# Optimization experiments

Measured on AMD Instinct MI355X. Metric: run time of the kernel, lower is better.

The kernel has to match this reference:

```python
import jax, jax.numpy as jnp
import numpy as np

IN_CH = 64
EMBED = 128
OUT_CH = 64
NUM_HEADS = 2
HEAD_DIM = EMBED // NUM_HEADS
B, D, H, W = 2, 16, 16, 16
SEQ = D * H * W


def setup_inputs() -> dict:
    key = jax.random.key(0)
    ks = jax.random.split(key, 12)
    s = lambda fan_in: 1.0 / np.sqrt(fan_in)
    return {
        "x": jax.random.normal(ks[0], (B, IN_CH, D, H, W), dtype=jnp.float32),
        "W_cp": jax.random.uniform(ks[1], (EMBED, IN_CH), jnp.float32, -s(IN_CH), s(IN_CH)),
        "b_cp": jax.random.uniform(ks[2], (EMBED,), jnp.float32, -s(IN_CH), s(IN_CH)),
        "W_q": jax.random.uniform(ks[3], (EMBED, EMBED), jnp.float32, -s(EMBED), s(EMBED)),
        "W_k": jax.random.uniform(ks[4], (EMBED, EMBED), jnp.float32, -s(EMBED), s(EMBED)),
        "W_v": jax.random.uniform(ks[5], (EMBED, EMBED), jnp.float32, -s(EMBED), s(EMBED)),
        "W_o": jax.random.uniform(ks[6], (EMBED, EMBED), jnp.float32, -s(EMBED), s(EMBED)),
        "b_o": jax.random.uniform(ks[7], (EMBED,), jnp.float32, -s(EMBED), s(EMBED)),
        "W_out": jax.random.uniform(ks[8], (OUT_CH, EMBED), jnp.float32, -s(EMBED), s(EMBED)),
        "b_out": jax.random.uniform(ks[9], (OUT_CH,), jnp.float32, -s(EMBED), s(EMBED)),
        "pos": jax.random.normal(ks[10], (1, SEQ, EMBED), dtype=jnp.float32) * 0.02,
        "gate": jnp.float32(0.1),
    }


def reference(x, W_cp, b_cp, W_q, W_k, W_v, W_o, b_o, W_out, b_out, pos, gate):
    b, c, d, h, w = x.shape
    seq = d * h * w
    scale = HEAD_DIM ** (-0.5)
    # (B, C, D, H, W) -> (B, S, C)
    xf = jnp.transpose(x, (0, 2, 3, 4, 1)).reshape(b, seq, c)
    xf = xf @ W_cp.T + b_cp + pos  # (B, S, E)
    # QKV projections, split heads: (B, nh, S, hd)
    def heads(t):
        return jnp.transpose(t.reshape(b, seq, NUM_HEADS, HEAD_DIM), (0, 2, 1, 3))
    q = heads(xf @ W_q.T)
    k = heads(xf @ W_k.T)
    v = heads(xf @ W_v.T)
    attn = jax.nn.softmax(jnp.einsum("bnsd,bntd->bnst", q, k) * scale, axis=-1)
    o = jnp.einsum("bnst,bntd->bnsd", attn, v)  # (B, nh, S, hd)
    o = jnp.transpose(o, (0, 2, 1, 3)).reshape(b, seq, EMBED)
    o = o @ W_o.T + b_o
    o = o @ W_out.T + b_out  # (B, S, out)
    out = jnp.transpose(o, (0, 2, 1)).reshape(b, OUT_CH, d, h, w)
    # in_channels == output_dim -> skip is identity (no conv/BN in original)
    return out + gate * x
```

## Files before the change

kernel.cpp:

```cpp
#include <hip/hip_runtime.h>
#include <hip/hip_bf16.h>
#include <cstdint>

typedef unsigned short u16;
typedef __attribute__((ext_vector_type(8))) short short8;
typedef __attribute__((ext_vector_type(4))) float f32x4;

#define MFMA(a, b, c) __builtin_amdgcn_mfma_f32_16x16x32_bf16((a), (b), (c), 0, 0, 0)

#define SEQ 4096
#define KSPLIT 8
#define NTILE (SEQ / KSPLIT / 32)

static __device__ __forceinline__ float b2f(u16 u) {
    union { float f; uint32_t i; } c; c.i = ((uint32_t)u) << 16; return c.f;
}
static __device__ __forceinline__ u16 f2b(float f) {
    union { float f; uint32_t i; } c; c.f = f;
    uint32_t r = c.i + 0x7FFF + ((c.i >> 16) & 1);
    return (u16)(r >> 16);
}
static __device__ __forceinline__ short8 ld8(const u16* p) {
    return *reinterpret_cast<const short8*>(p);
}
static __device__ __forceinline__ uint32_t pk2(float a, float b) {
    uint32_t r;
    asm("v_cvt_pk_bf16_f32 %0, %1, %2" : "=v"(r) : "v"(a), "v"(b));
    return r;
}
static __device__ __forceinline__ void gld16(const u16* g, u16* l) {
    __builtin_amdgcn_global_load_lds(
        (const __attribute__((address_space(1))) unsigned int*)g,
        (__attribute__((address_space(3))) unsigned int*)l, 16, 0, 0);
}

__global__ void k_prep(const float* __restrict__ Wo, const float* __restrict__ bo,
                       const float* __restrict__ Wout, const float* __restrict__ bout,
                       const float* __restrict__ Wcp, const float* __restrict__ Wq,
                       const float* __restrict__ Wk, const float* __restrict__ Wv,
                       u16* __restrict__ Wc, float* __restrict__ bc,
                       u16* __restrict__ Wcp_b, u16* __restrict__ Wq_b,
                       u16* __restrict__ Wk_b, u16* __restrict__ Wv_b) {
    int idx = blockIdx.x * 256 + threadIdx.x;
    if (idx < 8192) {
        int co = idx >> 7, e = idx & 127;
        float s = 0.f;
        for (int k = 0; k < 128; k++)
            s += Wout[co * 128 + k] * Wo[k * 128 + e];
        Wc[idx] = f2b(s);
    } else if (idx < 8256) {
        int co = idx - 8192;
        float s = bout[co];
        for (int k = 0; k < 128; k++)
            s += bo[k] * Wout[co * 128 + k];
        bc[co] = s;
    } else if (idx < 16448) {
        int i = idx - 8256;  Wcp_b[i] = f2b(Wcp[i]);
    } else if (idx < 32832) {
        int i = idx - 16448; Wq_b[i] = f2b(Wq[i]);
    } else if (idx < 49216) {
        int i = idx - 32832; Wk_b[i] = f2b(Wk[i]);
    } else if (idx < 65600) {
        int i = idx - 49216; Wv_b[i] = f2b(Wv[i]);
    }
}

__global__ __launch_bounds__(256) void k_front(const float* __restrict__ x,
                                               const u16* __restrict__ Wcp,
                                               const float* __restrict__ bcp,
                                               const float* __restrict__ pos,
                                               const u16* __restrict__ Wq,
                                               const u16* __restrict__ Wk,
                                               const u16* __restrict__ Wv,
                                               u16* __restrict__ Q, u16* __restrict__ K,
                                               u16* __restrict__ V) {
    __shared__ __align__(16) u16 xT[16][72];
    __shared__ __align__(16) u16 xfl[16 * 128];
    int blk = blockIdx.x;
    int b = blk >> 8, sb = (blk & 255) * 16;
    int t = threadIdx.x, w = t >> 6, l = t & 63, lc = l & 15, lg = l >> 4;

    {
        int c = t & 63, so = t >> 6;
        const float* src = x + ((size_t)b * 64 + c) * SEQ + sb + so * 4;
        f32x4 a0 = *reinterpret_cast<const f32x4*>(src);
#pragma unroll
        for (int j = 0; j < 4; j++) xT[so * 4 + j][c] = f2b(a0[j]);
    }
    __syncthreads();

    {
        short8 af[2];
        af[0] = ld8(&xT[lc][lg * 8]);
        af[1] = ld8(&xT[lc][32 + lg * 8]);
#pragma unroll
        for (int et = 0; et < 2; et++) {
            int nt = w * 2 + et;
            f32x4 acc = {0.f, 0.f, 0.f, 0.f};
#pragma unroll
            for (int ks = 0; ks < 2; ks++) {
                short8 bfr = ld8(Wcp + (nt * 16 + lc) * 64 + ks * 32 + lg * 8);
                acc = MFMA(af[ks], bfr, acc);
            }
            int e = nt * 16 + lc;
            float be = bcp[e];
            int chunk = e >> 3;
#pragma unroll
            for (int r = 0; r < 4; r++) {
                int sl = lg * 4 + r;
                float v = acc[r] + be + pos[(size_t)(sb + sl) * 128 + e];
                xfl[sl * 128 + ((chunk ^ (sl & 7)) << 3) + (e & 7)] = f2b(v);
            }
        }
    }
    __syncthreads();

    {
        short8 afq[4];
#pragma unroll
        for (int ks = 0; ks < 4; ks++)
            afq[ks] = ld8(&xfl[lc * 128 + (((ks * 4 + lg) ^ (lc & 7)) << 3)]);

        const float qscl = 0.18033688011112042f;
#pragma unroll
        for (int qk = 0; qk < 2; qk++) {
            const u16* W = qk ? Wk : Wq;
            u16* dst = qk ? K : Q;
#pragma unroll
            for (int et = 0; et < 2; et++) {
                int nt = w * 2 + et;
                f32x4 acc = {0.f, 0.f, 0.f, 0.f};
#pragma unroll
                for (int ks = 0; ks < 4; ks++) {
                    short8 bfr = ld8(W + (nt * 16 + lc) * 128 + ks * 32 + lg * 8);
                    acc = MFMA(afq[ks], bfr, acc);
                }
                int e = nt * 16 + lc, h = e >> 6, d = e & 63;
                float scl = qk ? 1.0f : qscl;
#pragma unroll
                for (int r = 0; r < 4; r++) {
                    int sr = sb + lg * 4 + r;
                    dst[(((size_t)b * 2 + h) * SEQ + sr) * 64 + d] = f2b(acc[r] * scl);
                }
            }
        }
#pragma unroll
        for (int et = 0; et < 2; et++) {
            int nt = w * 2 + et;
            f32x4 acc = {0.f, 0.f, 0.f, 0.f};
            short8 wv[4];
#pragma unroll
            for (int ks = 0; ks < 4; ks++)
                wv[ks] = ld8(Wv + (nt * 16 + lc) * 128 + ks * 32 + lg * 8);
#pragma unroll
            for (int ks = 0; ks < 4; ks++)
                acc = MFMA(wv[ks], afq[ks], acc);
#pragma unroll
            for (int r = 0; r < 4; r++) {
                int d = nt * 16 + lg * 4 + r, h = d >> 6, dd = d & 63;
                V[((size_t)(b * 2 + h) * 64 + dd) * SEQ + sb + lc] = f2b(acc[r]);
            }
        }
    }
}

__global__ __launch_bounds__(256, 4) void k_attn(const u16* __restrict__ Q,
                                                 const u16* __restrict__ K,
                                                 const u16* __restrict__ Vg,
                                                 u16* __restrict__ Op,
                                                 float2* __restrict__ ml) {
    __shared__ __align__(16) u16 Klds[2][2048];
    __shared__ __align__(16) u16 Vlds[2][2048];
    __shared__ __align__(16) u16 Pl[4][32][32];
    int blk = blockIdx.x;
    int split = blk >> 7, bh = (blk >> 5) & 3, qb = (blk & 31) * 128;
    int kbase = split * (SEQ / KSPLIT);
    const u16* Qp = Q + (size_t)bh * SEQ * 64;
    const u16* Kp = K + (size_t)bh * SEQ * 64;
    const u16* Vp = Vg + (size_t)bh * SEQ * 64;
    int t = threadIdx.x, w = t >> 6, l = t & 63, lc = l & 15, lg = l >> 4;
    uint32_t* plw = (uint32_t*)&Pl[w][0][0];
    const u16* plu = &Pl[w][0][0];

    const u16* kSrc = Kp + (size_t)(kbase + w * 8 + (l >> 3)) * 64 + (((l & 7) ^ (l >> 3)) << 3);
    int vrow = w * 16 + (l >> 2);
    int vswz = (l & 3) ^ ((((l >> 2) & 3) + (l >> 4)) & 3);
    const u16* vSrc = Vp + (size_t)vrow * SEQ + kbase + (vswz << 3);

    short8 qa[2][2];
#pragma unroll
    for (int ks = 0; ks < 2; ks++)
#pragma unroll
        for (int qh = 0; qh < 2; qh++)
            qa[ks][qh] = ld8(Qp + (size_t)(qb + w * 32 + qh * 16 + lc) * 64 + ks * 32 + lg * 8);

    short8 onesb;
#pragma unroll
    for (int i = 0; i < 8; i++) onesb[i] = (short)0x3F80;

    f32x4 oacc[2][4], lsacc[2];
#pragma unroll
    for (int qh = 0; qh < 2; qh++) {
        lsacc[qh] = (f32x4){0.f, 0.f, 0.f, 0.f};
#pragma unroll
        for (int dt = 0; dt < 4; dt++) oacc[qh][dt] = (f32x4){0.f, 0.f, 0.f, 0.f};
    }
    float m[2] = {-INFINITY, -INFINITY};

    int c0 = (lg ^ (lc & 7)) * 8;
    int sp = (((lc & 3) + (lc >> 2)) & 3);
    int cv = (lg ^ sp) * 8;

#define STAGE(buf, tt) do {                                       \
        gld16(kSrc + (size_t)(tt) * 2048, &Klds[buf][w * 512]);   \
        gld16(vSrc + (tt) * 32,           &Vlds[buf][w * 512]);   \
    } while (0)

    STAGE(0, 0);
    __syncthreads();

#pragma unroll 2
    for (int tt = 0; tt < NTILE; tt++) {
        int cur = tt & 1;
        if (tt + 1 < NTILE) STAGE(cur ^ 1, tt + 1);

        const u16* kb = Klds[cur];
        const u16* vb = Vlds[cur];

        f32x4 sc[2][2];
#pragma unroll
        for (int nt = 0; nt < 2; nt++) {
            short8 kf0 = ld8(kb + (nt * 16 + lc) * 64 + c0);
            short8 kf1 = ld8(kb + (nt * 16 + lc) * 64 + (c0 ^ 32));
#pragma unroll
            for (int qh = 0; qh < 2; qh++) {
                f32x4 a = {0.f, 0.f, 0.f, 0.f};
                a = MFMA(kf0, qa[0][qh], a);
                a = MFMA(kf1, qa[1][qh], a);
                sc[nt][qh] = a;
            }
        }

        float mx[2];
#pragma unroll
        for (int qh = 0; qh < 2; qh++)
            mx[qh] = fmaxf(
                fmaxf(fmaxf(sc[0][qh][0], sc[0][qh][1]), fmaxf(sc[0][qh][2], sc[0][qh][3])),
                fmaxf(fmaxf(sc[1][qh][0], sc[1][qh][1]), fmaxf(sc[1][qh][2], sc[1][qh][3])));

        if (__any((mx[0] - m[0] > 8.f) || (mx[1] - m[1] > 8.f))) {
#pragma unroll
            for (int qh = 0; qh < 2; qh++) {
                float mr = fmaxf(mx[qh], __shfl_xor(mx[qh], 16));
                mr = fmaxf(mr, __shfl_xor(mr, 32));
                float mn = fmaxf(m[qh], mr);
                float corr = exp2f(m[qh] - mn);
#pragma unroll
                for (int r = 0; r < 4; r++) {
                    float cr = __shfl(corr, lg * 4 + r);
#pragma unroll
                    for (int dt = 0; dt < 4; dt++) oacc[qh][dt][r] *= cr;
                    lsacc[qh][r] *= cr;
                }
                m[qh] = mn;
            }
        }

#pragma unroll
        for (int qh = 0; qh < 2; qh++) {
            int rowb = (qh * 16 + lc) * 16 + (lg & 1) * 2;
#pragma unroll
            for (int nt = 0; nt < 2; nt++) {
                uint2 u;
                u.x = pk2(exp2f(sc[nt][qh][0] - m[qh]), exp2f(sc[nt][qh][1] - m[qh]));
                u.y = pk2(exp2f(sc[nt][qh][2] - m[qh]), exp2f(sc[nt][qh][3] - m[qh]));
                int cc = (nt * 2 + (lg >> 1)) ^ sp;
                *reinterpret_cast<uint2*>(&plw[rowb + cc * 4]) = u;
            }
        }

        short8 pa0 = ld8(plu + (lc) * 32 + cv);
        short8 pa1 = ld8(plu + (16 + lc) * 32 + cv);
        lsacc[0] = MFMA(pa0, onesb, lsacc[0]);
        lsacc[1] = MFMA(pa1, onesb, lsacc[1]);
#pragma unroll
        for (int dt = 0; dt < 4; dt++) {
            short8 vf = ld8(vb + (dt * 16 + lc) * 32 + cv);
            oacc[0][dt] = MFMA(pa0, vf, oacc[0][dt]);
            oacc[1][dt] = MFMA(pa1, vf, oacc[1][dt]);
        }
        __syncthreads();
    }
#undef STAGE

    size_t rowbase = (size_t)(split * 4 + bh) * SEQ + qb + w * 32;
#pragma unroll
    for (int qh = 0; qh < 2; qh++)
#pragma unroll
        for (int dt = 0; dt < 4; dt++)
#pragma unroll
            for (int r = 0; r < 4; r++)
                Op[(rowbase + qh * 16 + lg * 4 + r) * 64 + dt * 16 + lc] = f2b(oacc[qh][dt][r]);
    float mr[2][4];
#pragma unroll
    for (int qh = 0; qh < 2; qh++)
#pragma unroll
        for (int r = 0; r < 4; r++) mr[qh][r] = __shfl(m[qh], lg * 4 + r);
    if (lc == 0) {
#pragma unroll
        for (int qh = 0; qh < 2; qh++)
#pragma unroll
            for (int r = 0; r < 4; r++) {
                float2 v; v.x = mr[qh][r]; v.y = lsacc[qh][r];
                ml[rowbase + qh * 16 + lg * 4 + r] = v;
            }
    }
}

__global__ __launch_bounds__(256) void k_back(const u16* __restrict__ Op,
                                              const float2* __restrict__ ml,
                                              const u16* __restrict__ Wc,
                                              const float* __restrict__ bc,
                                              const float* __restrict__ x,
                                              const float* __restrict__ gate,
                                              float* __restrict__ out) {
    __shared__ __align__(16) u16 Ol[16 * 128];
    int blk = blockIdx.x;
    int b = blk >> 8, sb = (blk & 255) * 16;
    int t = threadIdx.x, w = t >> 6, l = t & 63, lc = l & 15, lg = l >> 4;
    float g = gate[0];

    {
        int sl = t >> 4, ci = t & 15;
        int h = ci >> 3, d0 = (ci & 7) * 8;
        size_t rp0 = ((size_t)(b * 2 + h) << 12) + sb + sl;
        float2 e[KSPLIT];
        float ms = -INFINITY;
#pragma unroll
        for (int k = 0; k < KSPLIT; k++) {
            e[k] = ml[rp0 + (size_t)k * 16384];
            ms = fmaxf(ms, e[k].x);
        }
        float den = 0.f, c[KSPLIT];
#pragma unroll
        for (int k = 0; k < KSPLIT; k++) {
            c[k] = exp2f(e[k].x - ms);
            den += c[k] * e[k].y;
        }
        float inv = 1.0f / den;
        float acc[8];
#pragma unroll
        for (int j = 0; j < 8; j++) acc[j] = 0.f;
#pragma unroll
        for (int k = 0; k < KSPLIT; k++) {
            short8 a = ld8(Op + (rp0 + (size_t)k * 16384) * 64 + d0);
#pragma unroll
            for (int j = 0; j < 8; j++) acc[j] += c[k] * b2f((u16)a[j]);
        }
        short8 ov;
#pragma unroll
        for (int j = 0; j < 8; j++) ov[j] = (short)f2b(acc[j] * inv);
        *reinterpret_cast<short8*>(&Ol[sl * 128 + ((ci ^ (sl & 7)) << 3)]) = ov;
    }
    __syncthreads();

    short8 af[4];
#pragma unroll
    for (int ks = 0; ks < 4; ks++)
        af[ks] = ld8(Wc + (w * 16 + lc) * 128 + ks * 32 + lg * 8);

    f32x4 acc = {0.f, 0.f, 0.f, 0.f};
#pragma unroll
    for (int ks = 0; ks < 4; ks++) {
        short8 bfr = ld8(&Ol[lc * 128 + (((ks * 4 + lg) ^ (lc & 7)) << 3)]);
        acc = MFMA(af[ks], bfr, acc);
    }
#pragma unroll
    for (int r = 0; r < 4; r++) {
        int co = w * 16 + lg * 4 + r;
        int s = sb + lc;
        size_t idx = ((size_t)b * 64 + co) * SEQ + s;
        out[idx] = acc[r] + bc[co] + g * x[idx];
    }
}

extern "C" void kernel_launch(void* const* d_in, const int* in_sizes, int n_in,
                              void* d_out, int out_size, void* d_ws, size_t ws_size,
                              hipStream_t stream) {
    const float* x    = (const float*)d_in[0];
    const float* Wcp  = (const float*)d_in[1];
    const float* bcp  = (const float*)d_in[2];
    const float* Wq   = (const float*)d_in[3];
    const float* Wk   = (const float*)d_in[4];
    const float* Wv   = (const float*)d_in[5];
    const float* Wo   = (const float*)d_in[6];
    const float* bo   = (const float*)d_in[7];
    const float* Wout = (const float*)d_in[8];
    const float* bout = (const float*)d_in[9];
    const float* pos  = (const float*)d_in[10];
    const float* gate = (const float*)d_in[11];

    char* ws = (char*)d_ws;
    float2* mlp  = (float2*)(ws);
    u16*    Qb   = (u16*)(ws + (2u << 20));
    u16*    Kb   = (u16*)(ws + (4u << 20));
    u16*    Vt   = (u16*)(ws + (6u << 20));
    u16*    Wc   = (u16*)(ws + (10u << 20));
    float*  bc   = (float*)(ws + (10u << 20) + 16384);
    u16*    Wcp_b = (u16*)(ws + (10u << 20) + 32768);
    u16*    Wq_b  = (u16*)(ws + (10u << 20) + 49152);
    u16*    Wk_b  = (u16*)(ws + (10u << 20) + 81920);
    u16*    Wv_b  = (u16*)(ws + (10u << 20) + 114688);
    u16*    Opb  = (u16*)(ws + (10u << 20) + (512u << 10));
    float* out = (float*)d_out;

    hipLaunchKernelGGL(k_prep, dim3(257), dim3(256), 0, stream,
                       Wo, bo, Wout, bout, Wcp, Wq, Wk, Wv,
                       Wc, bc, Wcp_b, Wq_b, Wk_b, Wv_b);
    hipLaunchKernelGGL(k_front, dim3(512), dim3(256), 0, stream,
                       x, Wcp_b, bcp, pos, Wq_b, Wk_b, Wv_b, Qb, Kb, Vt);
    hipLaunchKernelGGL(k_attn, dim3(1024), dim3(256), 0, stream, Qb, Kb, Vt, Opb, mlp);
    hipLaunchKernelGGL(k_back, dim3(512), dim3(256), 0, stream, Opb, mlp, Wc, bc, x, gate, out);
}
```

Before: 61.96 us.

## Use 32x32 MFMA with transposed scores and permlane swaps instead of LDS P round-trip

Rewrites the attention inner loop to compute S^T with 32x32x16 bf16 MFMA, so each lane owns a single query row. The softmax max then needs one cross-half shuffle instead of row broadcasts. P is repacked into the next MFMA's operand layout with permlane32_swap in registers, removing the per-wave LDS write/read of P. The output is accumulated transposed and written as packed bf16 pairs. This changes the register layout and the swizzled LDS read patterns for K and V, which puts correctness and bank conflicts at risk.

New measurement: 61.76 us. Within noise of the previous version (-0.3%).

```diff
diff --git a/kernel.cpp b/kernel.cpp
--- a/kernel.cpp
+++ b/kernel.cpp
@@ -5,8 +5,10 @@
 typedef unsigned short u16;
 typedef __attribute__((ext_vector_type(8))) short short8;
 typedef __attribute__((ext_vector_type(4))) float f32x4;
+typedef __attribute__((ext_vector_type(16))) float f32x16;
 
 #define MFMA(a, b, c) __builtin_amdgcn_mfma_f32_16x16x32_bf16((a), (b), (c), 0, 0, 0)
+#define MFMA32(a, b, c) __builtin_amdgcn_mfma_f32_32x32x16_bf16((a), (b), (c), 0, 0, 0)
 
 #define SEQ 4096
 #define KSPLIT 8
@@ -27,6 +29,15 @@
     uint32_t r;
     asm("v_cvt_pk_bf16_f32 %0, %1, %2" : "=v"(r) : "v"(a), "v"(b));
     return r;
+}
+static __device__ __forceinline__ void plswap(uint32_t& a, uint32_t& b) {
+    typedef __attribute__((ext_vector_type(2))) unsigned int u32x2_;
+    u32x2_ r = __builtin_amdgcn_permlane32_swap(a, b, false, false);
+    a = r[0]; b = r[1];
+}
+static __device__ __forceinline__ short8 mk8(uint32_t a, uint32_t b, uint32_t c, uint32_t d) {
+    union { uint32_t u[4]; short8 s; } cv;
+    cv.u[0] = a; cv.u[1] = b; cv.u[2] = c; cv.u[3] = d; return cv.s;
 }
 static __device__ __forceinline__ void gld16(const u16* g, u16* l) {
     __builtin_amdgcn_global_load_lds(
@@ -171,45 +182,35 @@
                                                  float2* __restrict__ ml) {
     __shared__ __align__(16) u16 Klds[2][2048];
     __shared__ __align__(16) u16 Vlds[2][2048];
-    __shared__ __align__(16) u16 Pl[4][32][32];
     int blk = blockIdx.x;
     int split = blk >> 7, bh = (blk >> 5) & 3, qb = (blk & 31) * 128;
     int kbase = split * (SEQ / KSPLIT);
     const u16* Qp = Q + (size_t)bh * SEQ * 64;
     const u16* Kp = K + (size_t)bh * SEQ * 64;
     const u16* Vp = Vg + (size_t)bh * SEQ * 64;
-    int t = threadIdx.x, w = t >> 6, l = t & 63, lc = l & 15, lg = l >> 4;
-    uint32_t* plw = (uint32_t*)&Pl[w][0][0];
-    const u16* plu = &Pl[w][0][0];
+    int t = threadIdx.x, w = t >> 6, l = t & 63;
+    int q = l & 31, hi = l >> 5;
 
     const u16* kSrc = Kp + (size_t)(kbase + w * 8 + (l >> 3)) * 64 + (((l & 7) ^ (l >> 3)) << 3);
-    int vrow = w * 16 + (l >> 2);
     int vswz = (l & 3) ^ ((((l >> 2) & 3) + (l >> 4)) & 3);
-    const u16* vSrc = Vp + (size_t)vrow * SEQ + kbase + (vswz << 3);
-
-    short8 qa[2][2];
-#pragma unroll
-    for (int ks = 0; ks < 2; ks++)
-#pragma unroll
-        for (int qh = 0; qh < 2; qh++)
-            qa[ks][qh] = ld8(Qp + (size_t)(qb + w * 32 + qh * 16 + lc) * 64 + ks * 32 + lg * 8);
+    const u16* vSrc = Vp + (size_t)(w * 16 + (l >> 2)) * SEQ + kbase + (vswz << 3);
+
+    short8 qa[4];
+#pragma unroll
+    for (int c = 0; c < 4; c++)
+        qa[c] = ld8(Qp + (size_t)(qb + w * 32 + q) * 64 + c * 16 + hi * 8);
 
     short8 onesb;
 #pragma unroll
     for (int i = 0; i < 8; i++) onesb[i] = (short)0x3F80;
 
-    f32x4 oacc[2][4], lsacc[2];
-#pragma unroll
-    for (int qh = 0; qh < 2; qh++) {
-        lsacc[qh] = (f32x4){0.f, 0.f, 0.f, 0.f};
-#pragma unroll
-        for (int dt = 0; dt < 4; dt++) oacc[qh][dt] = (f32x4){0.f, 0.f, 0.f, 0.f};
-    }
-    float m[2] = {-INFINITY, -INFINITY};
-
-    int c0 = (lg ^ (lc & 7)) * 8;
-    int sp = (((lc & 3) + (lc >> 2)) & 3);
-    int cv = (lg ^ sp) * 8;
+    f32x16 oaccT[2], lsacc;
+#pragma unroll
+    for (int i = 0; i < 16; i++) { oaccT[0][i] = 0.f; oaccT[1][i] = 0.f; lsacc[i] = 0.f; }
+    float m = -INFINITY;
+
+    int kx = q & 7;
+    int sv = ((q & 3) + ((q >> 2) & 3)) & 3;
 
 #define STAGE(buf, tt) do {                                       \
         gld16(kSrc + (size_t)(tt) * 2048, &Klds[buf][w * 512]);   \
@@ -227,93 +228,68 @@
         const u16* kb = Klds[cur];
         const u16* vb = Vlds[cur];
 
-        f32x4 sc[2][2];
-#pragma unroll
-        for (int nt = 0; nt < 2; nt++) {
-            short8 kf0 = ld8(kb + (nt * 16 + lc) * 64 + c0);
-            short8 kf1 = ld8(kb + (nt * 16 + lc) * 64 + (c0 ^ 32));
-#pragma unroll
-            for (int qh = 0; qh < 2; qh++) {
-                f32x4 a = {0.f, 0.f, 0.f, 0.f};
-                a = MFMA(kf0, qa[0][qh], a);
-                a = MFMA(kf1, qa[1][qh], a);
-                sc[nt][qh] = a;
-            }
-        }
-
-        float mx[2];
-#pragma unroll
-        for (int qh = 0; qh < 2; qh++)
-            mx[qh] = fmaxf(
-                fmaxf(fmaxf(sc[0][qh][0], sc[0][qh][1]), fmaxf(sc[0][qh][2], sc[0][qh][3])),
-                fmaxf(fmaxf(sc[1][qh][0], sc[1][qh][1]), fmaxf(sc[1][qh][2], sc[1][qh][3])));
-
-        if (__any((mx[0] - m[0] > 8.f) || (mx[1] - m[1] > 8.f))) {
-#pragma unroll
-            for (int qh = 0; qh < 2; qh++) {
-                float mr = fmaxf(mx[qh], __shfl_xor(mx[qh], 16));
-                mr = fmaxf(mr, __shfl_xor(mr, 32));
-                float mn = fmaxf(m[qh], mr);
-                float corr = exp2f(m[qh] - mn);
-#pragma unroll
-                for (int r = 0; r < 4; r++) {
-                    float cr = __shfl(corr, lg * 4 + r);
-#pragma unroll
-                    for (int dt = 0; dt < 4; dt++) oacc[qh][dt][r] *= cr;
-                    lsacc[qh][r] *= cr;
-                }
-                m[qh] = mn;
-            }
-        }
-
-#pragma unroll
-        for (int qh = 0; qh < 2; qh++) {
-            int rowb = (qh * 16 + lc) * 16 + (lg & 1) * 2;
-#pragma unroll
-            for (int nt = 0; nt < 2; nt++) {
-                uint2 u;
-                u.x = pk2(exp2f(sc[nt][qh][0] - m[qh]), exp2f(sc[nt][qh][1] - m[qh]));
-                u.y = pk2(exp2f(sc[nt][qh][2] - m[qh]), exp2f(sc[nt][qh][3] - m[qh]));
-                int cc = (nt * 2 + (lg >> 1)) ^ sp;
-                *reinterpret_cast<uint2*>(&plw[rowb + cc * 4]) = u;
-            }
-        }
-
-        short8 pa0 = ld8(plu + (lc) * 32 + cv);
-        short8 pa1 = ld8(plu + (16 + lc) * 32 + cv);
-        lsacc[0] = MFMA(pa0, onesb, lsacc[0]);
-        lsacc[1] = MFMA(pa1, onesb, lsacc[1]);
-#pragma unroll
-        for (int dt = 0; dt < 4; dt++) {
-            short8 vf = ld8(vb + (dt * 16 + lc) * 32 + cv);
-            oacc[0][dt] = MFMA(pa0, vf, oacc[0][dt]);
-            oacc[1][dt] = MFMA(pa1, vf, oacc[1][dt]);
+        f32x16 sc;
+#pragma unroll
+        for (int i = 0; i < 16; i++) sc[i] = 0.f;
+#pragma unroll
+        for (int c = 0; c < 4; c++) {
+            short8 kf = ld8(kb + q * 64 + ((((c << 1) | hi) ^ kx) << 3));
+            sc = MFMA32(kf, qa[c], sc);
+        }
+
+        float mx = sc[0];
+#pragma unroll
+        for (int i = 1; i < 16; i++) mx = fmaxf(mx, sc[i]);
+        mx = fmaxf(mx, __shfl_xor(mx, 32));
+
+        if (__any(mx - m > 8.f)) {
+            float mn = fmaxf(m, mx);
+            float corr = exp2f(m - mn);
+#pragma unroll
+            for (int i = 0; i < 16; i++) { oaccT[0][i] *= corr; oaccT[1][i] *= corr; }
+            lsacc[0] *= corr;
+            m = mn;
+        }
+
+        float p[16];
+#pragma unroll
+        for (int i = 0; i < 16; i++) p[i] = exp2f(sc[i] - m);
+        uint32_t pk[8];
+#pragma unroll
+        for (int j = 0; j < 8; j++) pk[j] = pk2(p[2 * j], p[2 * j + 1]);
+
+        plswap(pk[0], pk[2]); plswap(pk[1], pk[3]);
+        plswap(pk[4], pk[6]); plswap(pk[5], pk[7]);
+        short8 pA0 = mk8(pk[0], pk[1], pk[2], pk[3]);
+        short8 pA1 = mk8(pk[4], pk[5], pk[6], pk[7]);
+
+        lsacc = MFMA32(onesb, pA0, lsacc);
+        lsacc = MFMA32(onesb, pA1, lsacc);
+
+#pragma unroll
+        for (int dt2 = 0; dt2 < 2; dt2++) {
+            short8 va0 = ld8(vb + (dt2 * 32 + q) * 32 + ((hi ^ sv) << 3));
+            short8 va1 = ld8(vb + (dt2 * 32 + q) * 32 + (((2 | hi) ^ sv) << 3));
+            oaccT[dt2] = MFMA32(va0, pA0, oaccT[dt2]);
+            oaccT[dt2] = MFMA32(va1, pA1, oaccT[dt2]);
         }
         __syncthreads();
     }
 #undef STAGE
 
-    size_t rowbase = (size_t)(split * 4 + bh) * SEQ + qb + w * 32;
-#pragma unroll
-    for (int qh = 0; qh < 2; qh++)
-#pragma unroll
-        for (int dt = 0; dt < 4; dt++)
-#pragma unroll
-            for (int r = 0; r < 4; r++)
-                Op[(rowbase + qh * 16 + lg * 4 + r) * 64 + dt * 16 + lc] = f2b(oacc[qh][dt][r]);
-    float mr[2][4];
-#pragma unroll
-    for (int qh = 0; qh < 2; qh++)
-#pragma unroll
-        for (int r = 0; r < 4; r++) mr[qh][r] = __shfl(m[qh], lg * 4 + r);
-    if (lc == 0) {
-#pragma unroll
-        for (int qh = 0; qh < 2; qh++)
-#pragma unroll
-            for (int r = 0; r < 4; r++) {
-                float2 v; v.x = mr[qh][r]; v.y = lsacc[qh][r];
-                ml[rowbase + qh * 16 + lg * 4 + r] = v;
-            }
+    size_t rowbase = (size_t)(split * 4 + bh) * SEQ + qb + w * 32 + q;
+    u16* orow = Op + rowbase * 64;
+#pragma unroll
+    for (int dt2 = 0; dt2 < 2; dt2++)
+#pragma unroll
+        for (int i = 0; i < 16; i += 2) {
+            int d = dt2 * 32 + (i & 3) + 8 * (i >> 2) + 4 * hi;
+            uint32_t wv = pk2(oaccT[dt2][i], oaccT[dt2][i + 1]);
+            *reinterpret_cast<uint32_t*>(orow + d) = wv;
+        }
+    if (hi == 0) {
+        float2 v; v.x = m; v.y = lsacc[0];
+        ml[rowbase] = v;
     }
 }
 
```
